# Optimization experiments

Hardware: AMD Instinct MI355X
Metric: run time of the kernel (lower is better)

Reference implementation:

```python
import jax, jax.numpy as jnp
import numpy as np

B, N, HW, PS, FHW = 16, 4096, 224, 8, 56

def _gelu(x):
    return jax.nn.gelu(x, approximate=True)  # tanh approximation, matches nn.GELU(approximate='tanh')

def _conv(x, w, b, stride):
    y = jax.lax.conv_general_dilated(x, w, (stride, stride), [(1, 1), (1, 1)],
                                     dimension_numbers=('NCHW', 'OIHW', 'NCHW'))
    return y + b[None, :, None, None]

def _embed(points):
    # for i in 0..11: append sin(2^i * p) then cos(2^i * p) -> [B,N,48]
    factors = 2.0 ** jnp.arange(12, dtype=points.dtype)
    scaled = points[..., None, :] * factors[:, None]          # [B,N,12,2]
    feats = jnp.concatenate([jnp.sin(scaled), jnp.cos(scaled)], axis=-1)  # [B,N,12,4]
    return feats.reshape(points.shape[0], points.shape[1], 48)

def _extract_patches(fmap, points):
    # fmap [B,C,H,W]; points in [0,1]; bilinear grid_sample, zeros padding, align_corners=True
    Bq, C, H, W = fmap.shape
    centers = points * 2.0 - 1.0
    step = 2.0 / (W - 1)
    half = (PS - 1) / 2.0
    offs = jnp.linspace(-half, half, PS, dtype=fmap.dtype) * step
    offx2d, offy2d = jnp.meshgrid(offs, offs, indexing='ij')   # [ps,ps]
    gx = centers[..., 0][..., None, None] + offx2d             # [B,N,ps,ps]
    gy = centers[..., 1][..., None, None] + offy2d
    # align_corners=True pixel coords
    ix = (gx + 1.0) * 0.5 * (W - 1)
    iy = (gy + 1.0) * 0.5 * (H - 1)
    x0f = jnp.floor(ix); y0f = jnp.floor(iy)
    x0 = x0f.astype(jnp.int32); y0 = y0f.astype(jnp.int32)
    x1 = x0 + 1; y1 = y0 + 1
    wx1 = ix - x0f; wx0 = 1.0 - wx1
    wy1 = iy - y0f; wy0 = 1.0 - wy1
    fflat = fmap.reshape(Bq, C, H * W)

    def corner(xi, yi, w):
        valid = ((xi >= 0) & (xi < W) & (yi >= 0) & (yi < H)).astype(fmap.dtype)
        idx = jnp.clip(yi, 0, H - 1) * W + jnp.clip(xi, 0, W - 1)   # [B,N,ps,ps]
        vals = jax.vmap(lambda f, i: f[:, i])(fflat, idx)           # [B,C,N,ps,ps]
        return vals * (w * valid)[:, None]

    out = (corner(x0, y0, wx0 * wy0) + corner(x1, y0, wx1 * wy0)
           + corner(x0, y1, wx0 * wy1) + corner(x1, y1, wx1 * wy1))  # [B,C,N,ps,ps]
    return out.transpose(0, 2, 1, 3, 4)                              # [B,N,C,ps,ps]

def setup_inputs():
    key = jax.random.key(0)
    ks = jax.random.split(key, 26)
    def w(k, shape):
        fan_in = int(np.prod(shape[1:]))
        return jax.random.normal(k, shape, jnp.float32) * (1.0 / np.sqrt(fan_in))
    inp = {
        'points': jax.random.uniform(ks[0], (B, N, 2), jnp.float32),
        'images': jax.random.normal(ks[1], (B, 3, HW, HW), jnp.float32),
        # plane encoder
        'pw1': w(ks[2], (16, 3, 3, 3)),  'pb1': jnp.zeros((16,), jnp.float32),
        'pw2': w(ks[3], (32, 16, 3, 3)), 'pb2': jnp.zeros((32,), jnp.float32),
        'pw3': w(ks[4], (4, 32, 3, 3)),  'pb3': jnp.zeros((4,), jnp.float32),
        # global encoder
        'gw1': w(ks[5], (4, 3, 3, 3)),   'gb1': jnp.zeros((4,), jnp.float32),
        'gw2': w(ks[6], (8, 4, 3, 3)),   'gb2': jnp.zeros((8,), jnp.float32),
        'gw3': w(ks[7], (16, 8, 3, 3)),  'gb3': jnp.zeros((16,), jnp.float32),
        'gw4': w(ks[8], (32, 16, 3, 3)), 'gb4': jnp.zeros((32,), jnp.float32),
        'gw5': w(ks[9], (64, 32, 3, 3)), 'gb5': jnp.zeros((64,), jnp.float32),
        # point encoder (torch Linear: [out,in])
        'lw1': w(ks[10], (256, 48)),  'lb1': jnp.zeros((256,), jnp.float32),
        'lw2': w(ks[11], (256, 256)), 'lb2': jnp.zeros((256,), jnp.float32),
        # head
        'hw1': w(ks[12], (512, 576)), 'hb1': jnp.zeros((512,), jnp.float32),
        'hw2': w(ks[13], (1, 512)),   'hb2': jnp.zeros((1,), jnp.float32),
    }
    return inp

def reference(points, images, pw1, pb1, pw2, pb2, pw3, pb3,
              gw1, gb1, gw2, gb2, gw3, gb3, gw4, gb4, gw5, gb5,
              lw1, lb1, lw2, lb2, hw1, hb1, hw2, hb2):
    # point branch
    pe = _embed(points)                                         # [B,N,48]
    pf = _gelu(pe @ lw1.T + lb1) @ lw2.T + lb2                  # [B,N,256]
    # plane encoder -> 4x56x56 fmap
    f = _gelu(_conv(images, pw1, pb1, 2))
    f = _gelu(_conv(f, pw2, pb2, 2))
    fmap = _gelu(_conv(f, pw3, pb3, 1))                         # [B,4,56,56]
    # global encoder -> [B,64]
    g = images
    for wg, bg in ((gw1, gb1), (gw2, gb2), (gw3, gb3), (gw4, gb4), (gw5, gb5)):
        g = _gelu(_conv(g, wg, bg, 2))
    gc = g.mean(axis=(2, 3))                                    # AvgPool2d(7)+Flatten -> [B,64]
    gc = jnp.broadcast_to(gc[:, None, :], (points.shape[0], points.shape[1], 64))
    # per-point bilinear patch gather
    patches = _extract_patches(fmap, points).reshape(points.shape[0], points.shape[1], -1)  # [B,N,256]
    fused = jnp.concatenate([pf, patches, gc], axis=-1)         # [B,N,576]
    logit = _gelu(fused @ hw1.T + hb1) @ hw2.T + hb2            # [B,N,1]
    return logit
```

## Files before the change

kernel.cpp:

```cpp
#include <hip/hip_runtime.h>
#include <math.h>

#define BB 16
#define NN 4096
#define M_TOT (BB*NN)
#define HBK 64

typedef __attribute__((ext_vector_type(8))) short s8v;
typedef __attribute__((ext_vector_type(4))) float f4v;

__device__ __forceinline__ float gelu_t(float x){
    float u = 1.5957691216057308f * x * (1.0f + 0.044715f*x*x);
    return x / (1.0f + __expf(-u));
}

__device__ __forceinline__ unsigned short f2bf(float f){
    unsigned int u = __float_as_uint(f);
    u += 0x7fffu + ((u >> 16) & 1u);
    return (unsigned short)(u >> 16);
}

#define GLL(src, dst) __builtin_amdgcn_global_load_lds( \
    (const __attribute__((address_space(1))) void*)(src), \
    (__attribute__((address_space(3))) void*)(dst), 16, 0, 0)

template<int CIN, int COUT, int STRIDE, int CHUNK>
__device__ __forceinline__ void conv_dev2(
    const float* __restrict__ in, const float* __restrict__ w,
    const float* __restrict__ bias, float* __restrict__ out,
    int Hin, int Win, int Hout, int Wout, int bx, int by, int b, float* tile)
{
    constexpr int IW = 15*STRIDE + 3;
    constexpr int IH = IW;
    constexpr int PITCH = IW + 1;
    int tid = threadIdx.x;
    int tx = tid & 15, ty = tid >> 4;
    int wo = bx*16 + tx;
    int ho = by*16 + ty;
    int win0 = bx*16*STRIDE - 1;
    int hin0 = by*16*STRIDE - 1;
    bool valid = (wo < Wout) && (ho < Hout);

    float acc[COUT];
    #pragma unroll
    for (int co = 0; co < COUT; ++co) acc[co] = bias[co];

    const float* ib = in + (size_t)(b*CIN)*Hin*Win;
    for (int ci0 = 0; ci0 < CIN; ci0 += CHUNK) {
        __syncthreads();
        for (int idx = tid; idx < CHUNK*IH*IW; idx += 256) {
            int c = idx / (IH*IW), rem = idx - c*(IH*IW);
            int r = rem / IW, cc = rem - r*IW;
            int hi = hin0 + r, wi = win0 + cc;
            float v = 0.f;
            if ((unsigned)hi < (unsigned)Hin && (unsigned)wi < (unsigned)Win)
                v = ib[(size_t)(ci0 + c)*Hin*Win + hi*Win + wi];
            tile[c*IH*PITCH + r*PITCH + cc] = v;
        }
        __syncthreads();
        for (int ci = 0; ci < CHUNK; ++ci) {
            float vv[9];
            const float* tb = tile + ci*IH*PITCH;
            #pragma unroll
            for (int kh = 0; kh < 3; ++kh)
                #pragma unroll
                for (int kw = 0; kw < 3; ++kw)
                    vv[kh*3+kw] = tb[(ty*STRIDE + kh)*PITCH + tx*STRIDE + kw];
            const float* wc = w + (ci0 + ci)*9;
            #pragma unroll
            for (int co = 0; co < COUT; ++co) {
                const float* wp = wc + co*CIN*9;
                #pragma unroll
                for (int k = 0; k < 9; ++k)
                    acc[co] = fmaf(vv[k], wp[k], acc[co]);
            }
        }
    }
    if (valid) {
        size_t obase = ((size_t)b*COUT)*Hout*Wout + (size_t)ho*Wout + wo;
        #pragma unroll
        for (int co = 0; co < COUT; ++co)
            out[obase + (size_t)co*Hout*Wout] = gelu_t(acc[co]);
    }
}

__global__ __launch_bounds__(256) void conv_dual_k(
    const float* __restrict__ in,
    const float* __restrict__ wA, const float* __restrict__ bA,
    const float* __restrict__ wB, const float* __restrict__ bB,
    float* __restrict__ outA, float* __restrict__ outB)
{
    __shared__ float tile[3*33*34];
    const int Hin = 224, Win = 224, Hout = 112, Wout = 112;
    int tid = threadIdx.x;
    int tx = tid & 15, ty = tid >> 4;
    int b = blockIdx.z;
    int wo = blockIdx.x*16 + tx;
    int ho = blockIdx.y*16 + ty;
    int win0 = blockIdx.x*32 - 1;
    int hin0 = blockIdx.y*32 - 1;

    const float* ib = in + (size_t)(b*3)*Hin*Win;
    for (int idx = tid; idx < 3*1089; idx += 256) {
        int c = idx / 1089, rem = idx - c*1089;
        int r = rem / 33, cc = rem - r*33;
        int hi = hin0 + r, wi = win0 + cc;
        float v = 0.f;
        if ((unsigned)hi < (unsigned)Hin && (unsigned)wi < (unsigned)Win)
            v = ib[(size_t)c*Hin*Win + hi*Win + wi];
        tile[c*33*34 + r*34 + cc] = v;
    }
    __syncthreads();

    float accA[16], accB[4];
    #pragma unroll
    for (int co = 0; co < 16; ++co) accA[co] = bA[co];
    #pragma unroll
    for (int co = 0; co < 4; ++co) accB[co] = bB[co];

    #pragma unroll
    for (int ci = 0; ci < 3; ++ci) {
        float vv[9];
        const float* tb = tile + ci*33*34;
        #pragma unroll
        for (int kh = 0; kh < 3; ++kh)
            #pragma unroll
            for (int kw = 0; kw < 3; ++kw)
                vv[kh*3+kw] = tb[(ty*2 + kh)*34 + tx*2 + kw];
        #pragma unroll
        for (int co = 0; co < 16; ++co) {
            const float* wp = wA + co*27 + ci*9;
            #pragma unroll
            for (int k = 0; k < 9; ++k) accA[co] = fmaf(vv[k], wp[k], accA[co]);
        }
        #pragma unroll
        for (int co = 0; co < 4; ++co) {
            const float* wp = wB + co*27 + ci*9;
            #pragma unroll
            for (int k = 0; k < 9; ++k) accB[co] = fmaf(vv[k], wp[k], accB[co]);
        }
    }
    size_t px = (size_t)ho*Wout + wo;
    #pragma unroll
    for (int co = 0; co < 16; ++co)
        outA[((size_t)(b*16 + co))*Hout*Wout + px] = gelu_t(accA[co]);
    #pragma unroll
    for (int co = 0; co < 4; ++co)
        outB[((size_t)(b*4 + co))*Hout*Wout + px] = gelu_t(accB[co]);
}

__global__ __launch_bounds__(256) void conv_pg2_k(
    const float* __restrict__ f1, const float* __restrict__ pw2, const float* __restrict__ pb2, float* __restrict__ f2,
    const float* __restrict__ g1, const float* __restrict__ gw2, const float* __restrict__ gb2, float* __restrict__ g2)
{
    __shared__ float tile[8*33*34];
    int z = blockIdx.z;
    if (z < 32) {
        int b = z >> 1, half = z & 1;
        conv_dev2<16,16,2,8>(f1 + (size_t)b*16*12544, pw2 + half*2304, pb2 + half*16,
                             f2 + ((size_t)(b*32 + half*16))*3136,
                             112,112, 56,56, blockIdx.x, blockIdx.y, 0, tile);
    } else {
        conv_dev2<4,8,2,4>(g1, gw2, gb2, g2, 112,112, 56,56, blockIdx.x, blockIdx.y, z-32, tile);
    }
}

__global__ __launch_bounds__(256) void conv_pg3_k(
    const float* __restrict__ f2, const float* __restrict__ pw3, const float* __restrict__ pb3, float4* __restrict__ fmap4,
    const float* __restrict__ g2, const float* __restrict__ gw3, const float* __restrict__ gb3, float* __restrict__ g3)
{
    __shared__ float tile[8*33*34];
    int z = blockIdx.z;
    if (z < 16) {
        int b = z;
        int idx = blockIdx.x*256 + threadIdx.x;
        if (idx >= 3136) return;
        int ho = idx / 56, wo = idx - ho*56;
        const float* ib = f2 + (size_t)b*32*3136;
        float acc[4];
        #pragma unroll
        for (int co = 0; co < 4; ++co) acc[co] = pb3[co];
        for (int ci = 0; ci < 32; ++ci) {
            const float* ic = ib + (size_t)ci*3136;
            #pragma unroll
            for (int kh = 0; kh < 3; ++kh) {
                int hi = ho - 1 + kh;
                if ((unsigned)hi >= 56u) continue;
                #pragma unroll
                for (int kw = 0; kw < 3; ++kw) {
                    int wi = wo - 1 + kw;
                    if ((unsigned)wi >= 56u) continue;
                    float v = ic[hi*56 + wi];
                    int wofs = ci*9 + kh*3 + kw;
                    #pragma unroll
                    for (int co = 0; co < 4; ++co)
                        acc[co] = fmaf(v, pw3[co*288 + wofs], acc[co]);
                }
            }
        }
        float4 o;
        o.x = gelu_t(acc[0]); o.y = gelu_t(acc[1]);
        o.z = gelu_t(acc[2]); o.w = gelu_t(acc[3]);
        fmap4[(size_t)b*3136 + idx] = o;
    } else {
        if (blockIdx.x >= 4) return;
        int bx = blockIdx.x & 1, by = blockIdx.x >> 1;
        conv_dev2<8,16,2,8>(g2, gw3, gb3, g3, 56,56, 28,28, bx, by, z-16, tile);
    }
}

__global__ __launch_bounds__(256) void k4_k(
    const float* __restrict__ g3, const float* __restrict__ w4,
    const float* __restrict__ b4, float* __restrict__ g4o,
    const float4* __restrict__ fmap4, const float* __restrict__ points,
    unsigned short* __restrict__ C)
{
    __shared__ float4 pt[4*81];
    int bid = blockIdx.x;
    int tid = threadIdx.x;
    if (bid < 392) {
        int idx = bid*256 + tid;
        int co = idx & 31;
        int t = idx >> 5;
        int b = t / 196, px = t - b*196;
        int ho = px / 14, wo = px - ho*14;
        const float* src = g3 + (size_t)b*16*784;
        const float* wp = w4 + co*144;
        float acc = b4[co];
        for (int ci = 0; ci < 16; ++ci) {
            #pragma unroll
            for (int kh = 0; kh < 3; ++kh) {
                int hi = ho*2 - 1 + kh;
                if ((unsigned)hi >= 28u) continue;
                #pragma unroll
                for (int kw = 0; kw < 3; ++kw) {
                    int wi = wo*2 - 1 + kw;
                    if ((unsigned)wi >= 28u) continue;
                    acc = fmaf(src[ci*784 + hi*28 + wi], wp[ci*9 + kh*3 + kw], acc);
                }
            }
        }
        g4o[(size_t)b*6272 + px*32 + co] = gelu_t(acc);
    } else {
        int task = (bid - 392)*256 + tid;
        int wv = tid >> 6, lane = tid & 63;
        size_t m = (size_t)(task >> 6);
        int ij = task & 63;
        int i = ij >> 3, j = ij & 7;
        int b = (int)(m >> 12);
        float px = points[m*2], py = points[m*2+1];
        float X = fmaf(px, 55.f, -3.5f);
        float Y = fmaf(py, 55.f, -3.5f);
        float xbf = floorf(X), ybf = floorf(Y);
        int xbase = (int)xbf, ybase = (int)ybf;
        float wx1 = X - xbf, wx0 = 1.f - wx1;
        float wy1 = Y - ybf, wy0 = 1.f - wy1;
        const float4* fb = fmap4 + (size_t)b*3136;
        float4* tp = pt + wv*81;

        {
            int r = lane / 9, c = lane - r*9;
            int y = ybase + r, x = xbase + c;
            float4 v = {0.f, 0.f, 0.f, 0.f};
            if ((unsigned)x < 56u && (unsigned)y < 56u) v = fb[y*56 + x];
            tp[lane] = v;
            int idx2 = 64 + lane;
            if (idx2 < 81) {
                int r2 = idx2 / 9, c2 = idx2 - r2*9;
                int y2 = ybase + r2, x2 = xbase + c2;
                float4 v2 = {0.f, 0.f, 0.f, 0.f};
                if ((unsigned)x2 < 56u && (unsigned)y2 < 56u) v2 = fb[y2*56 + x2];
                tp[idx2] = v2;
            }
        }
        __syncthreads();

        float4 f00 = tp[j*9 + i];
        float4 f10 = tp[j*9 + i + 1];
        float4 f01 = tp[j*9 + 9 + i];
        float4 f11 = tp[j*9 + 9 + i + 1];
        float4 v;
        v.x = wy0*(wx0*f00.x + wx1*f10.x) + wy1*(wx0*f01.x + wx1*f11.x);
        v.y = wy0*(wx0*f00.y + wx1*f10.y) + wy1*(wx0*f01.y + wx1*f11.y);
        v.z = wy0*(wx0*f00.z + wx1*f10.z) + wy1*(wx0*f01.z + wx1*f11.z);
        v.w = wy0*(wx0*f00.w + wx1*f10.w) + wy1*(wx0*f01.w + wx1*f11.w);
        ushort4 o;
        o.x = f2bf(v.x); o.y = f2bf(v.y); o.z = f2bf(v.z); o.w = f2bf(v.w);
        *(ushort4*)(C + m*512 + 256 + ij*4) = o;
    }
}

__global__ __launch_bounds__(256) void g5_k(
    const float* __restrict__ g4o, const float* __restrict__ w5,
    const float* __restrict__ b5, float* __restrict__ gc)
{
    int idx = blockIdx.x*256 + threadIdx.x;
    int co = idx & 63;
    int t = idx >> 6;
    int b = t / 49, px = t - b*49;
    int ho = px / 7, wo = px - ho*7;
    const float* src = g4o + (size_t)b*6272;
    const float* wp = w5 + co*288;
    float acc = b5[co];
    for (int ci = 0; ci < 32; ++ci) {
        #pragma unroll
        for (int kh = 0; kh < 3; ++kh) {
            int hi = ho*2 - 1 + kh;
            if ((unsigned)hi >= 14u) continue;
            #pragma unroll
            for (int kw = 0; kw < 3; ++kw) {
                int wi = wo*2 - 1 + kw;
                if ((unsigned)wi >= 14u) continue;
                acc = fmaf(src[(hi*14 + wi)*32 + ci], wp[ci*9 + kh*3 + kw], acc);
            }
        }
    }
    atomicAdd(&gc[b*64 + co], gelu_t(acc) * (1.0f/49.0f));
}

__global__ __launch_bounds__(256) void hgc_k(
    const float* __restrict__ gc, const float* __restrict__ hw1,
    const float* __restrict__ hb1, float* __restrict__ hgc)
{
    int idx = blockIdx.x*256 + threadIdx.x;
    int b = idx >> 9, n = idx & 511;
    const float* g = gc + b*64;
    const float* w = hw1 + (size_t)n*576 + 512;
    float s = hb1[n];
    #pragma unroll
    for (int c = 0; c < 64; ++c) s = fmaf(g[c], w[c], s);
    hgc[idx] = s;
}

__global__ void cvtall_k(const float* __restrict__ lw1, const float* __restrict__ lw2,
                         const float* __restrict__ hw1, unsigned short* __restrict__ blw1,
                         unsigned short* __restrict__ blw2, unsigned short* __restrict__ bhw1,
                         float* __restrict__ out, const float* __restrict__ b2,
                         float* __restrict__ gc){
    int i = blockIdx.x*blockDim.x + threadIdx.x;
    if (i < M_TOT) out[i] = b2[0];
    if (i < 1024) gc[i] = 0.f;
    if (i < 256*64) {
        int r = i >> 6, c = i & 63;
        blw1[i] = (c < 48) ? f2bf(lw1[r*48 + c]) : 0;
        return;
    }
    int j = i - 256*64;
    if (j < 256*256) { blw2[j] = f2bf(lw2[j]); return; }
    j -= 256*256;
    if (j < 512*576) {
        int n = j / 576, k = j - n*576;
        int src_k = k;
        if (k >= 256 && k < 512) {
            int s = k - 256;
            src_k = 256 + (s & 3)*64 + (s >> 2);
        }
        bhw1[j] = f2bf(hw1[(size_t)n*576 + src_k]);
    }
}

__global__ __launch_bounds__(512) void mlp12_k(
    const float* __restrict__ points,
    const unsigned short* __restrict__ W1, const float* __restrict__ b1,
    const unsigned short* __restrict__ W2, const float* __restrict__ b2,
    unsigned short* __restrict__ C)
{
    __shared__ unsigned short Pe[128*64];
    __shared__ unsigned short Hd[128*256];
    int tid = threadIdx.x;
    int wv = tid >> 6, lane = tid & 63;
    int q = lane >> 4, lr = lane & 15;
    int mi = wv >> 2, ni = wv & 3;
    size_t m0 = (size_t)blockIdx.x * 128;

    #pragma unroll
    for (int it = 0; it < 2; ++it) {
        int idx = it*512 + tid;
        int row = idx >> 3, seg = idx & 7;
        size_t m = m0 + row;
        float px = points[m*2], py = points[m*2+1];
        union { s8v v; unsigned short u[8]; } pk;
        #pragma unroll
        for (int j = 0; j < 8; ++j) {
            int k = seg*8 + j;
            unsigned short val = 0;
            if (k < 48) {
                int i2 = k >> 2, rr = k & 3;
                float f = (float)(1 << i2);
                float p = (rr & 1) ? py : px;
                float s = f * p;
                val = f2bf((rr < 2) ? __sinf(s) : __cosf(s));
            }
            pk.u[j] = val;
        }
        *(s8v*)(Pe + (row*8 + (seg ^ (row & 7)))*8) = pk.v;
    }
    __syncthreads();

    f4v acc1[4][4];
    #pragma unroll
    for (int i = 0; i < 4; ++i)
        #pragma unroll
        for (int j = 0; j < 4; ++j) acc1[i][j] = (f4v){0.f,0.f,0.f,0.f};

    #pragma unroll
    for (int kb = 0; kb < 2; ++kb) {
        int seg = kb*4 + q;
        s8v a[4], b[4];
        #pragma unroll
        for (int t = 0; t < 4; ++t) {
            int row = mi*64 + t*16 + lr;
            a[t] = *(const s8v*)(Pe + (row*8 + (seg ^ (row & 7)))*8);
        }
        #pragma unroll
        for (int t = 0; t < 4; ++t) {
            int n = ni*64 + t*16 + lr;
            b[t] = *(const s8v*)(W1 + n*64 + seg*8);
        }
        #pragma unroll
        for (int mt = 0; mt < 4; ++mt)
            #pragma unroll
            for (int nt = 0; nt < 4; ++nt)
                acc1[mt][nt] = __builtin_amdgcn_mfma_f32_16x16x32_bf16(a[mt], b[nt], acc1[mt][nt], 0, 0, 0);
    }
    {
        float b1v[4];
        #pragma unroll
        for (int nt = 0; nt < 4; ++nt) b1v[nt] = b1[ni*64 + nt*16 + lr];
        #pragma unroll
        for (int mt = 0; mt < 4; ++mt)
            #pragma unroll
            for (int r4 = 0; r4 < 4; ++r4) {
                int row = mi*64 + mt*16 + q*4 + r4;
                #pragma unroll
                for (int nt = 0; nt < 4; ++nt) {
                    int col = ni*64 + nt*16 + lr;
                    float v = gelu_t(acc1[mt][nt][r4] + b1v[nt]);
                    int p = (col >> 3) ^ (row & 7);
                    Hd[(row*32 + p)*8 + (col & 7)] = f2bf(v);
                }
            }
    }
    __syncthreads();

    f4v acc2[4][4];
    #pragma unroll
    for (int i = 0; i < 4; ++i)
        #pragma unroll
        for (int j = 0; j < 4; ++j) acc2[i][j] = (f4v){0.f,0.f,0.f,0.f};

    #pragma unroll 2
    for (int kt = 0; kt < 8; ++kt) {
        s8v a[4], b[4];
        #pragma unroll
        for (int t = 0; t < 4; ++t) {
            int n = ni*64 + t*16 + lr;
            b[t] = *(const s8v*)(W2 + (size_t)n*256 + kt*32 + q*8);
        }
        #pragma unroll
        for (int t = 0; t < 4; ++t) {
            int row = mi*64 + t*16 + lr;
            int p = (kt*4 + q) ^ (row & 7);
            a[t] = *(const s8v*)(Hd + (row*32 + p)*8);
        }
        #pragma unroll
        for (int mt = 0; mt < 4; ++mt)
            #pragma unroll
            for (int nt = 0; nt < 4; ++nt)
                acc2[mt][nt] = __builtin_amdgcn_mfma_f32_16x16x32_bf16(a[mt], b[nt], acc2[mt][nt], 0, 0, 0);
    }
    {
        float b2v[4];
        #pragma unroll
        for (int nt = 0; nt < 4; ++nt) b2v[nt] = b2[ni*64 + nt*16 + lr];
        #pragma unroll
        for (int mt = 0; mt < 4; ++mt)
            #pragma unroll
            for (int r4 = 0; r4 < 4; ++r4) {
                size_t m = m0 + mi*64 + mt*16 + q*4 + r4;
                #pragma unroll
                for (int nt = 0; nt < 4; ++nt) {
                    int n = ni*64 + nt*16 + lr;
                    C[m*512 + n] = f2bf(acc2[mt][nt][r4] + b2v[nt]);
                }
            }
    }
}

__global__ __launch_bounds__(256, 2) void gemm_hd_k(
    const unsigned short* __restrict__ A,
    const unsigned short* __restrict__ W,
    const float* __restrict__ hgc, const float* __restrict__ w2,
    float* __restrict__ out)
{
    __shared__ unsigned short As[2][64*HBK];
    __shared__ unsigned short Bs[2][256*HBK];
    int tid = threadIdx.x;
    int wv = tid >> 6, lane = tid & 63;
    int q = lane >> 4, lr = lane & 15;
    int nq = wv * 64;
    size_t m0 = (size_t)blockIdx.x * 64;
    int nbase = blockIdx.y * 256;
    int bimg = (int)(m0 >> 12);

    const unsigned short* srcA[2]; int dA[2];
    #pragma unroll
    for (int r = 0; r < 2; ++r) {
        int f = r*256 + tid;
        int row = f >> 3, sl = (f & 7) ^ (row & 7);
        srcA[r] = A + (m0 + row)*512 + sl*8;
        dA[r] = f*8;
    }
    const unsigned short* srcB[8]; int dB[8];
    #pragma unroll
    for (int r = 0; r < 8; ++r) {
        int f = r*256 + tid;
        int row = f >> 3, sl = (f & 7) ^ (row & 7);
        srcB[r] = W + (size_t)(nbase + row)*576 + sl*8;
        dB[r] = f*8;
    }

    f4v acc[4][4];
    #pragma unroll
    for (int i = 0; i < 4; ++i)
        #pragma unroll
        for (int j = 0; j < 4; ++j) acc[i][j] = (f4v){0.f,0.f,0.f,0.f};

    auto STAGE = [&](int buf) {
        #pragma unroll
        for (int r = 0; r < 2; ++r) { GLL(srcA[r], &As[buf][dA[r]]); srcA[r] += HBK; }
        #pragma unroll
        for (int r = 0; r < 8; ++r) { GLL(srcB[r], &Bs[buf][dB[r]]); srcB[r] += HBK; }
    };
    auto COMPUTE = [&](int buf) {
        #pragma unroll
        for (int kk = 0; kk < 2; ++kk) {
            s8v a[4], b[4];
            #pragma unroll
            for (int t = 0; t < 4; ++t) {
                int row = t*16 + lr;
                int ph = (kk*4 + q) ^ (row & 7);
                a[t] = *(const s8v*)(&As[buf][(row*8 + ph)*8]);
            }
            #pragma unroll
            for (int t = 0; t < 4; ++t) {
                int row = nq + t*16 + lr;
                int ph = (kk*4 + q) ^ (row & 7);
                b[t] = *(const s8v*)(&Bs[buf][(row*8 + ph)*8]);
            }
            #pragma unroll
            for (int mt = 0; mt < 4; ++mt)
                #pragma unroll
                for (int nt = 0; nt < 4; ++nt)
                    acc[mt][nt] = __builtin_amdgcn_mfma_f32_16x16x32_bf16(a[mt], b[nt], acc[mt][nt], 0, 0, 0);
        }
    };

    STAGE(0);
    #pragma unroll 1
    for (int t = 0; t < 3; ++t) {
        __syncthreads(); STAGE(1); COMPUTE(0);
        __syncthreads(); STAGE(0); COMPUTE(1);
    }
    __syncthreads(); STAGE(1); COMPUTE(0);
    __syncthreads();            COMPUTE(1);

    float bv[4], w2v[4];
    #pragma unroll
    for (int nt = 0; nt < 4; ++nt) {
        int n = nbase + nq + nt*16 + lr;
        bv[nt] = hgc[bimg*512 + n];
        w2v[nt] = w2[n];
    }
    __syncthreads();
    float* red = (float*)&As[0][0];
    #pragma unroll
    for (int mt = 0; mt < 4; ++mt)
        #pragma unroll
        for (int r4 = 0; r4 < 4; ++r4) {
            int ml = mt*16 + q*4 + r4;
            float s = 0.f;
            #pragma unroll
            for (int nt = 0; nt < 4; ++nt)
                s += gelu_t(acc[mt][nt][r4] + bv[nt]) * w2v[nt];
            #pragma unroll
            for (int off = 8; off > 0; off >>= 1) s += __shfl_down(s, off, 16);
            if (lr == 0) red[wv*64 + ml] = s;
        }
    __syncthreads();
    if (tid < 64) {
        float t = red[tid] + red[64 + tid] + red[128 + tid] + red[192 + tid];
        atomicAdd(&out[m0 + tid], t);
    }
}

extern "C" void kernel_launch(void* const* d_in, const int* in_sizes, int n_in,
                              void* d_out, int out_size, void* d_ws, size_t ws_size,
                              hipStream_t stream) {
    const float* points = (const float*)d_in[0];
    const float* images = (const float*)d_in[1];
    const float* pw1 = (const float*)d_in[2];  const float* pb1 = (const float*)d_in[3];
    const float* pw2 = (const float*)d_in[4];  const float* pb2 = (const float*)d_in[5];
    const float* pw3 = (const float*)d_in[6];  const float* pb3 = (const float*)d_in[7];
    const float* gw1 = (const float*)d_in[8];  const float* gb1 = (const float*)d_in[9];
    const float* gw2 = (const float*)d_in[10]; const float* gb2 = (const float*)d_in[11];
    const float* gw3 = (const float*)d_in[12]; const float* gb3 = (const float*)d_in[13];
    const float* gw4 = (const float*)d_in[14]; const float* gb4 = (const float*)d_in[15];
    const float* gw5 = (const float*)d_in[16]; const float* gb5 = (const float*)d_in[17];
    const float* lw1 = (const float*)d_in[18]; const float* lb1 = (const float*)d_in[19];
    const float* lw2 = (const float*)d_in[20]; const float* lb2 = (const float*)d_in[21];
    const float* hw1 = (const float*)d_in[22]; const float* hb1 = (const float*)d_in[23];
    const float* hw2 = (const float*)d_in[24]; const float* hb2 = (const float*)d_in[25];
    float* out = (float*)d_out;

    char* base = (char*)d_ws;
    unsigned short* fused_b = (unsigned short*)base;
    float4* fmap4 = (float4*)(fused_b + (size_t)M_TOT*512);
    float* g3   = (float*)(fmap4 + (size_t)16*3136);
    float* g4o  = g3 + (size_t)16*16*784;
    float* gc   = g4o + (size_t)16*32*196;
    float* hgc  = gc + 1024;
    unsigned short* blw1 = (unsigned short*)(hgc + 16*512);
    unsigned short* blw2 = blw1 + 256*64;
    unsigned short* bhw1 = blw2 + 256*256;
    float* ct = (float*)base;
    float* f1 = ct;
    float* f2 = f1 + (size_t)16*16*112*112;
    float* g1 = f2 + (size_t)16*32*56*56;
    float* g2 = g1 + (size_t)16*4*112*112;

    cvtall_k<<<1472, 256, 0, stream>>>(lw1, lw2, hw1, blw1, blw2, bhw1, out, hb2, gc);
    conv_dual_k<<<dim3(7,7,16), 256, 0, stream>>>(images, pw1, pb1, gw1, gb1, f1, g1);
    conv_pg2_k<<<dim3(4,4,48), 256, 0, stream>>>(f1, pw2, pb2, f2, g1, gw2, gb2, g2);
    conv_pg3_k<<<dim3(13,1,32), 256, 0, stream>>>(f2, pw3, pb3, fmap4, g2, gw3, gb3, g3);
    k4_k<<<392 + 16384, 256, 0, stream>>>(g3, gw4, gb4, g4o, fmap4, points, fused_b);
    g5_k<<<196, 256, 0, stream>>>(g4o, gw5, gb5, gc);
    hgc_k<<<32, 256, 0, stream>>>(gc, hw1, hb1, hgc);
    mlp12_k<<<M_TOT/128, 512, 0, stream>>>(points, blw1, lb1, blw2, lb2, fused_b);
    gemm_hd_k<<<dim3(M_TOT/64, 2), 256, 0, stream>>>(fused_b, bhw1, hgc, hw2, out);
}
```

Baseline: 403.7 us.

## Enlarge head GEMM tile to 128 rows with 8 waves and explicit pipeline

The final head GEMM now uses 512-thread blocks with a 2x4 wave grid covering a 128x256 tile, so each block loads the weight tile once for twice as many rows. The K loop is fully unrolled with explicit vmcnt waits, raw s_barrier, sched_barrier and setprio around the MFMA compute. LDS offsets are precomputed, and bias/w2 loads are hoisted before the loop. This roughly halves weight traffic per output row and aims to overlap loads with MFMA better, at the cost of more LDS per block (a separate reduction buffer) and possibly lower occupancy.

```diff
diff --git a/kernel.cpp b/kernel.cpp
--- a/kernel.cpp
+++ b/kernel.cpp
@@ -4,7 +4,6 @@
 #define BB 16
 #define NN 4096
 #define M_TOT (BB*NN)
-#define HBK 64
 
 typedef __attribute__((ext_vector_type(8))) short s8v;
 typedef __attribute__((ext_vector_type(4))) float f4v;
@@ -487,67 +486,81 @@
     }
 }
 
-__global__ __launch_bounds__(256, 2) void gemm_hd_k(
+__global__ __launch_bounds__(512, 2) void gemm_hd_k(
     const unsigned short* __restrict__ A,
     const unsigned short* __restrict__ W,
     const float* __restrict__ hgc, const float* __restrict__ w2,
     float* __restrict__ out)
 {
-    __shared__ unsigned short As[2][64*HBK];
-    __shared__ unsigned short Bs[2][256*HBK];
+    __shared__ unsigned short As[2][128*64];
+    __shared__ unsigned short Bs[2][256*64];
+    __shared__ float red[8*64];
     int tid = threadIdx.x;
     int wv = tid >> 6, lane = tid & 63;
     int q = lane >> 4, lr = lane & 15;
-    int nq = wv * 64;
-    size_t m0 = (size_t)blockIdx.x * 64;
+    int wm = wv >> 2, wn = wv & 3;
+    size_t m0 = (size_t)blockIdx.x * 128;
     int nbase = blockIdx.y * 256;
     int bimg = (int)(m0 >> 12);
 
+    float bv[4], w2v[4];
+    #pragma unroll
+    for (int nt = 0; nt < 4; ++nt) {
+        int n = nbase + wn*64 + nt*16 + lr;
+        bv[nt] = hgc[bimg*512 + n];
+        w2v[nt] = w2[n];
+    }
+    asm volatile("s_waitcnt vmcnt(0)" ::: "memory");
+
     const unsigned short* srcA[2]; int dA[2];
     #pragma unroll
     for (int r = 0; r < 2; ++r) {
-        int f = r*256 + tid;
+        int f = r*512 + tid;
         int row = f >> 3, sl = (f & 7) ^ (row & 7);
         srcA[r] = A + (m0 + row)*512 + sl*8;
         dA[r] = f*8;
     }
-    const unsigned short* srcB[8]; int dB[8];
-    #pragma unroll
-    for (int r = 0; r < 8; ++r) {
-        int f = r*256 + tid;
+    const unsigned short* srcB[4]; int dB[4];
+    #pragma unroll
+    for (int r = 0; r < 4; ++r) {
+        int f = r*512 + tid;
         int row = f >> 3, sl = (f & 7) ^ (row & 7);
         srcB[r] = W + (size_t)(nbase + row)*576 + sl*8;
         dB[r] = f*8;
     }
 
+    int aoff[2][4], boff[2][4];
+    #pragma unroll
+    for (int kk = 0; kk < 2; ++kk) {
+        #pragma unroll
+        for (int t = 0; t < 4; ++t) {
+            int rowA = wm*64 + t*16 + lr;
+            aoff[kk][t] = (rowA*8 + ((kk*4 + q) ^ (rowA & 7)))*8;
+            int rowB = wn*64 + t*16 + lr;
+            boff[kk][t] = (rowB*8 + ((kk*4 + q) ^ (rowB & 7)))*8;
+        }
+    }
+
     f4v acc[4][4];
     #pragma unroll
     for (int i = 0; i < 4; ++i)
         #pragma unroll
         for (int j = 0; j < 4; ++j) acc[i][j] = (f4v){0.f,0.f,0.f,0.f};
 
-    auto STAGE = [&](int buf) {
-        #pragma unroll
-        for (int r = 0; r < 2; ++r) { GLL(srcA[r], &As[buf][dA[r]]); srcA[r] += HBK; }
-        #pragma unroll
-        for (int r = 0; r < 8; ++r) { GLL(srcB[r], &Bs[buf][dB[r]]); srcB[r] += HBK; }
+    auto STAGE = [&](int buf, int ks) {
+        #pragma unroll
+        for (int r = 0; r < 2; ++r) GLL(srcA[r] + ks*64, &As[buf][dA[r]]);
+        #pragma unroll
+        for (int r = 0; r < 4; ++r) GLL(srcB[r] + ks*64, &Bs[buf][dB[r]]);
     };
     auto COMPUTE = [&](int buf) {
         #pragma unroll
         for (int kk = 0; kk < 2; ++kk) {
             s8v a[4], b[4];
             #pragma unroll
-            for (int t = 0; t < 4; ++t) {
-                int row = t*16 + lr;
-                int ph = (kk*4 + q) ^ (row & 7);
-                a[t] = *(const s8v*)(&As[buf][(row*8 + ph)*8]);
-            }
-            #pragma unroll
-            for (int t = 0; t < 4; ++t) {
-                int row = nq + t*16 + lr;
-                int ph = (kk*4 + q) ^ (row & 7);
-                b[t] = *(const s8v*)(&Bs[buf][(row*8 + ph)*8]);
-            }
+            for (int t = 0; t < 4; ++t) a[t] = *(const s8v*)(&As[buf][aoff[kk][t]]);
+            #pragma unroll
+            for (int t = 0; t < 4; ++t) b[t] = *(const s8v*)(&Bs[buf][boff[kk][t]]);
             #pragma unroll
             for (int mt = 0; mt < 4; ++mt)
                 #pragma unroll
@@ -556,24 +569,26 @@
         }
     };
 
-    STAGE(0);
-    #pragma unroll 1
-    for (int t = 0; t < 3; ++t) {
-        __syncthreads(); STAGE(1); COMPUTE(0);
-        __syncthreads(); STAGE(0); COMPUTE(1);
-    }
-    __syncthreads(); STAGE(1); COMPUTE(0);
-    __syncthreads();            COMPUTE(1);
-
-    float bv[4], w2v[4];
-    #pragma unroll
-    for (int nt = 0; nt < 4; ++nt) {
-        int n = nbase + nq + nt*16 + lr;
-        bv[nt] = hgc[bimg*512 + n];
-        w2v[nt] = w2[n];
-    }
-    __syncthreads();
-    float* red = (float*)&As[0][0];
+    STAGE(0, 0);
+    #pragma unroll
+    for (int t = 0; t < 8; ++t) {
+        const int cur = t & 1;
+        if (t < 7) {
+            STAGE(cur ^ 1, t + 1);
+            asm volatile("s_waitcnt vmcnt(6)" ::: "memory");
+        } else {
+            asm volatile("s_waitcnt vmcnt(0)" ::: "memory");
+        }
+        __builtin_amdgcn_s_barrier();
+        __builtin_amdgcn_sched_barrier(0);
+        __builtin_amdgcn_s_setprio(1);
+        COMPUTE(cur);
+        __builtin_amdgcn_s_setprio(0);
+        __builtin_amdgcn_sched_barrier(0);
+        __builtin_amdgcn_s_barrier();
+        __builtin_amdgcn_sched_barrier(0);
+    }
+
     #pragma unroll
     for (int mt = 0; mt < 4; ++mt)
         #pragma unroll
@@ -588,8 +603,10 @@
             if (lr == 0) red[wv*64 + ml] = s;
         }
     __syncthreads();
-    if (tid < 64) {
-        float t = red[tid] + red[64 + tid] + red[128 + tid] + red[192 + tid];
+    if (tid < 128) {
+        int wmI = tid >> 6, ml = tid & 63;
+        float t = red[(wmI*4 + 0)*64 + ml] + red[(wmI*4 + 1)*64 + ml]
+                + red[(wmI*4 + 2)*64 + ml] + red[(wmI*4 + 3)*64 + ml];
         atomicAdd(&out[m0 + tid], t);
     }
 }
@@ -637,5 +654,5 @@
     g5_k<<<196, 256, 0, stream>>>(g4o, gw5, gb5, gc);
     hgc_k<<<32, 256, 0, stream>>>(gc, hw1, hb1, hgc);
     mlp12_k<<<M_TOT/128, 512, 0, stream>>>(points, blw1, lb1, blw2, lb2, fused_b);
-    gemm_hd_k<<<dim3(M_TOT/64, 2), 256, 0, stream>>>(fused_b, bhw1, hgc, hw2, out);
-}
+    gemm_hd_k<<<dim3(M_TOT/128, 2), 512, 0, stream>>>(fused_b, bhw1, hgc, hw2, out);
+}
```

Measured after the change: 405.7 us. No clear change (+0.5%).
